# Performance work log

Hardware: AMD Instinct MI355X
Metric: run time of the kernel (lower is better)

The kernel has to match this reference:

```python
import jax, jax.numpy as jnp
import numpy as np

TEMPERATURE = 0.07
MSE_WEIGHT = 0.5
SUPCON_WEIGHT = 1.0
EPS = 1e-12  # F.normalize default eps

P_POS = 4000
P_NEG = 4000
NVOX = 32768
FEAT = 128


def setup_inputs() -> dict:
    key = jax.random.key(0)
    k1, k2, k3, k4, k5 = jax.random.split(key, 5)
    Zs = jax.random.normal(k1, (1, FEAT, NVOX), dtype=jnp.float32)
    pos_idx = jax.random.randint(k2, (P_POS,), 0, NVOX, dtype=jnp.int32)
    neg_idx = jax.random.randint(k3, (P_NEG,), 0, NVOX, dtype=jnp.int32)
    feature_diff = jax.random.normal(k4, (1, FEAT, 32, 32, 32), dtype=jnp.float32)
    input_diff = jax.random.normal(k5, (1, FEAT, 32, 32, 32), dtype=jnp.float32)
    return {"Zs": Zs, "pos_idx": pos_idx, "neg_idx": neg_idx,
            "feature_diff": feature_diff, "input_diff": input_diff}


def _l2_normalize_rows(x):
    # F.normalize(x, dim=1): x / max(||x||_2, eps)
    n = jnp.sqrt(jnp.sum(x * x, axis=1, keepdims=True))
    return x / jnp.maximum(n, EPS)


def _supcon_loss(Zs, pos_idx, neg_idx):
    feats = Zs[0].T                                   # [Nvox, F]
    pixels = jnp.concatenate([feats[pos_idx], feats[neg_idx]], axis=0)  # [N, F]
    n = pixels.shape[0]
    labels = jnp.concatenate([jnp.ones((P_POS,), jnp.int32),
                              jnp.zeros((P_NEG,), jnp.int32)])
    pixels = _l2_normalize_rows(pixels)
    dot = jnp.matmul(pixels, pixels.T) / TEMPERATURE  # [N, N]
    dot = _l2_normalize_rows(dot)                     # row-normalize the NxN matrix
    expm = jnp.exp(dot)
    class_mask = (labels[:, None] == labels[None, :]) & ~jnp.eye(n, dtype=bool)
    pos_term = expm * class_mask
    pos_term = jnp.where(pos_term == 0, 1.0, pos_term)
    denom = jnp.sum(expm * ~class_mask, axis=1) - jnp.diagonal(expm)  # [N]
    full_term = jnp.log(pos_term) - jnp.log(denom)[None, :]
    return -(1.0 / n) * jnp.sum(full_term)


def reference(Zs, pos_idx, neg_idx, feature_diff, input_diff):
    supcon = _supcon_loss(Zs, pos_idx, neg_idx)
    mse = jnp.mean((feature_diff - input_diff) ** 2)
    return SUPCON_WEIGHT * supcon + MSE_WEIGHT * mse
```

## Files before the change

### kernel.cpp

```cpp
#include <hip/hip_runtime.h>
#include <hip/hip_bf16.h>
#include <math.h>

typedef unsigned short u16;
typedef float  f32x4  __attribute__((ext_vector_type(4)));
typedef __bf16 bf16x8 __attribute__((ext_vector_type(8)));

#define NPOS   4000
#define LDP    136
#define TILE_CH 2176
#define MSE_N  4194304
#define GATHER_B 256
#define MSE_B    512
#define TLD    132

__device__ __forceinline__ void load_lds16(const void* g, void* l) {
  __builtin_amdgcn_global_load_lds(
      (const __attribute__((address_space(1))) unsigned int*)g,
      (__attribute__((address_space(3))) unsigned int*)l, 16, 0, 0);
}

__device__ __forceinline__ float bf2f(u16 h) {
  unsigned u = ((unsigned)h) << 16;
  return __builtin_bit_cast(float, u);
}

struct Args {
  const float* Zs; const int* pos; const int* neg;
  const float4* fd; const float4* idf;
  u16* Pc; u16* Prow; float* G; float* S;
  float* qpos; float* qneg; float* sdpos; float* sdneg;
  float* msepart; float* out;
};

__global__ __launch_bounds__(256) void prep_k(Args a) {
  __shared__ __align__(16) float tile[128 * TLD];
  __shared__ int mlist[1024];
  __shared__ int mcnt;
  int blk = blockIdx.x, tid = threadIdx.x;
  int wave = tid >> 6, lane = tid & 63;
  if (blk < GATHER_B) {
    int v0 = blk << 7;
    if (tid == 0) mcnt = 0;
    __syncthreads();
    {
      int rq = tid >> 5;
      int c4 = (tid & 31) << 2;
      #pragma unroll
      for (int p = 0; p < 16; ++p) {
        int f = p * 8 + rq;
        float4 v = *(const float4*)(a.Zs + ((size_t)f << 15) + v0 + c4);
        *(float4*)&tile[f * TLD + c4] = v;
      }
    }
    for (int k = 0; k < 4000; k += 256) {
      int i = k + tid;
      if (i < 4000) {
        unsigned dp = (unsigned)(a.pos[i] - v0);
        if (dp < 128u) { int m = atomicAdd(&mcnt, 1); mlist[m] = (i << 7) | dp; }
        unsigned dn = (unsigned)(a.neg[i] - v0);
        if (dn < 128u) { int m = atomicAdd(&mcnt, 1); mlist[m] = ((4096 + i) << 7) | dn; }
      }
    }
    __syncthreads();
    int nm = mcnt;
    for (int m = wave; m < nm; m += 4) {
      int e = mlist[m];
      int col = e >> 7, lv = e & 127;
      float x0 = tile[lane * TLD + lv];
      float x1 = tile[(lane + 64) * TLD + lv];
      float s = x0 * x0 + x1 * x1;
      #pragma unroll
      for (int o = 1; o < 64; o <<= 1) s += __shfl_xor(s, o, 64);
      float inv = 1.0f / fmaxf(sqrtf(s), 1e-12f);
      __hip_bfloat16 h0 = __float2bfloat16(x0 * inv);
      __hip_bfloat16 h1 = __float2bfloat16(x1 * inv);
      u16 b0 = *(u16*)&h0, b1 = *(u16*)&h1;
      a.Prow[(size_t)col * LDP + lane]      = b0;
      a.Prow[(size_t)col * LDP + lane + 64] = b1;
      size_t cbase = (size_t)(col >> 7) * (128 * LDP) + (col & 127);
      a.Pc[cbase + (size_t)lane * LDP]        = b0;
      a.Pc[cbase + (size_t)(lane + 64) * LDP] = b1;
    }
  } else if (blk < GATHER_B + MSE_B) {
    int b = blk - GATHER_B;
    float ms = 0.f;
    for (int idx = b * 256 + tid; idx < MSE_N / 4; idx += MSE_B * 256) {
      float4 u = a.fd[idx], w = a.idf[idx];
      float dx = u.x - w.x, dy = u.y - w.y, dz = u.z - w.z, dv = u.w - w.w;
      ms += dx * dx + dy * dy + dz * dz + dv * dv;
    }
    #pragma unroll
    for (int o = 1; o < 64; o <<= 1) ms += __shfl_xor(ms, o, 64);
    __shared__ float red[4];
    if (lane == 0) red[wave] = ms;
    __syncthreads();
    if (tid == 0) a.msepart[b] = red[0] + red[1] + red[2] + red[3];
  } else if (blk < GATHER_B + MSE_B + 2) {
    int ch = (blk == GATHER_B + MSE_B) ? 31 : 63;
    for (int e = tid; e < 128 * 96; e += 256) {
      int f = e / 96, c = 32 + e % 96;
      a.Pc[(size_t)ch * (128 * LDP) + (size_t)f * LDP + c] = 0;
    }
  } else {
    int b = blk - (GATHER_B + MSE_B + 2);
    float4 z = {0.f, 0.f, 0.f, 0.f};
    for (int i = b * 256 + tid; i < 8256; i += 512) ((float4*)a.G)[i] = z;
  }
}

__global__ __launch_bounds__(256) void syrk_k(Args a) {
  __shared__ __align__(16) u16 T0[128 * LDP];
  int blk = blockIdx.x, tid = threadIdx.x;
  int wave = tid >> 6, lane = tid & 63;
  int wm = (wave >> 1) << 6, wn = (wave & 1) << 6;
  int r = lane & 15, q = lane >> 4;
  int sf = tid >> 1, sh = tid & 1;
  float ssum = 0.f;
  f32x4 acc[4][4];
  #pragma unroll
  for (int x = 0; x < 4; ++x)
    #pragma unroll
    for (int y = 0; y < 4; ++y) {
      acc[x][y][0] = 0.f; acc[x][y][1] = 0.f; acc[x][y][2] = 0.f; acc[x][y][3] = 0.f;
    }
  for (int it = 0; it < 4; ++it) {
    const u16* g = a.Pc + (size_t)(blk * 4 + it) * (128 * LDP);
    #pragma unroll
    for (int k = 0; k < 9; ++k) {
      int cc = k * 256 + tid;
      if (cc < TILE_CH) load_lds16(g + cc * 8, &T0[cc * 8]);
    }
    __syncthreads();
    #pragma unroll
    for (int kk = 0; kk < 4; ++kk) {
      int k0 = kk * 32 + q * 8;
      bf16x8 af[4], bfr[4];
      #pragma unroll
      for (int t = 0; t < 4; ++t) {
        af[t]  = *(const bf16x8*)&T0[(wm + t * 16 + r) * LDP + k0];
        bfr[t] = *(const bf16x8*)&T0[(wn + t * 16 + r) * LDP + k0];
      }
      #pragma unroll
      for (int mt = 0; mt < 4; ++mt)
        #pragma unroll
        for (int nt = 0; nt < 4; ++nt)
          acc[mt][nt] = __builtin_amdgcn_mfma_f32_16x16x32_bf16(
              af[mt], bfr[nt], acc[mt][nt], 0, 0, 0);
    }
    {
      const u16* base = &T0[sf * LDP + sh * 64];
      #pragma unroll
      for (int vb = 0; vb < 8; ++vb) {
        bf16x8 v = *(const bf16x8*)&base[vb * 8];
        #pragma unroll
        for (int j = 0; j < 8; ++j) ssum += (float)v[j];
      }
    }
    __syncthreads();
  }
  float* Gf = a.G + (size_t)(blk >> 3) * 16384;
  #pragma unroll
  for (int mt = 0; mt < 4; ++mt)
    #pragma unroll
    for (int nt = 0; nt < 4; ++nt)
      #pragma unroll
      for (int reg = 0; reg < 4; ++reg) {
        int ar = wm + mt * 16 + q * 4 + reg;
        int bc = wn + nt * 16 + r;
        atomicAdd(&Gf[ar * 128 + bc], acc[mt][nt][reg]);
      }
  ssum += __shfl_xor(ssum, 1, 64);
  if (sh == 0) atomicAdd(&a.S[(blk >> 3) * 128 + sf], ssum);
}

__global__ __launch_bounds__(256) void quad_k(Args a) {
  __shared__ __align__(16) u16 T0[128 * LDP];
  __shared__ __align__(16) u16 T1[128 * LDP];
  __shared__ float Sl[256];
  __shared__ float qld[2][128];
  int cb = blockIdx.x & 63, set = blockIdx.x >> 6, tid = threadIdx.x;
  Sl[tid] = a.S[tid];
  const u16* gP = a.Prow + (size_t)cb * (128 * LDP);
  #pragma unroll
  for (int k = 0; k < 9; ++k) {
    int cc = k * 256 + tid;
    if (cc < TILE_CH) load_lds16(gP + cc * 8, &T1[cc * 8]);
  }
  {
    int f = tid >> 1, half = (tid & 1) * 64;
    const float4* gsrc = (const float4*)(a.G + (size_t)set * 16384 + f * 128 + half);
    #pragma unroll
    for (int j16 = 0; j16 < 16; ++j16) {
      float4 v = gsrc[j16];
      __hip_bfloat16 c0 = __float2bfloat16(v.x), c1 = __float2bfloat16(v.y);
      __hip_bfloat16 c2 = __float2bfloat16(v.z), c3 = __float2bfloat16(v.w);
      ushort4 pk = { *(u16*)&c0, *(u16*)&c1, *(u16*)&c2, *(u16*)&c3 };
      *(ushort4*)&T0[f * LDP + half + j16 * 4] = pk;
    }
  }
  __syncthreads();
  int wave = tid >> 6, lane = tid & 63;
  int wm = (wave >> 1) << 6, wn = (wave & 1) << 6;
  int r = lane & 15, q = lane >> 4;
  f32x4 acc[4][4];
  #pragma unroll
  for (int x = 0; x < 4; ++x)
    #pragma unroll
    for (int y = 0; y < 4; ++y) {
      acc[x][y][0] = 0.f; acc[x][y][1] = 0.f; acc[x][y][2] = 0.f; acc[x][y][3] = 0.f;
    }
  #pragma unroll
  for (int kk = 0; kk < 4; ++kk) {
    int k0 = kk * 32 + q * 8;
    bf16x8 af[4], bfr[4];
    #pragma unroll
    for (int t = 0; t < 4; ++t) {
      af[t]  = *(const bf16x8*)&T0[(wm + t * 16 + r) * LDP + k0];
      bfr[t] = *(const bf16x8*)&T1[(wn + t * 16 + r) * LDP + k0];
    }
    #pragma unroll
    for (int mt = 0; mt < 4; ++mt)
      #pragma unroll
      for (int nt = 0; nt < 4; ++nt)
        acc[mt][nt] = __builtin_amdgcn_mfma_f32_16x16x32_bf16(
            af[mt], bfr[nt], acc[mt][nt], 0, 0, 0);
  }
  float qv[4] = {0.f, 0.f, 0.f, 0.f};
  #pragma unroll
  for (int nt = 0; nt < 4; ++nt) {
    int il = wn + nt * 16 + r;
    #pragma unroll
    for (int mt = 0; mt < 4; ++mt) {
      const u16* pp = &T1[il * LDP + wm + mt * 16 + q * 4];
      #pragma unroll
      for (int reg = 0; reg < 4; ++reg)
        qv[nt] += acc[mt][nt][reg] * bf2f(pp[reg]);
    }
  }
  #pragma unroll
  for (int nt = 0; nt < 4; ++nt) {
    qv[nt] += __shfl_xor(qv[nt], 16, 64);
    qv[nt] += __shfl_xor(qv[nt], 32, 64);
  }
  int half = wm >> 6;
  if (q == 0) {
    #pragma unroll
    for (int nt = 0; nt < 4; ++nt) qld[half][wn + nt * 16 + r] = qv[nt];
  }
  __syncthreads();
  float* qarr = set ? a.qneg : a.qpos;
  if (tid < 128) qarr[cb * 128 + tid] = qld[0][tid] + qld[1][tid];
  if (set == 0) {
    int which = tid >> 7, sl = tid & 127;
    const float* Sv = &Sl[which * 128];
    float d = 0.f;
    #pragma unroll
    for (int fb = 0; fb < 16; ++fb) {
      const u16* pv = &T1[sl * LDP + fb * 8];
      #pragma unroll
      for (int j = 0; j < 8; ++j) d += Sv[fb * 8 + j] * bf2f(pv[j]);
    }
    (which ? a.sdneg : a.sdpos)[cb * 128 + sl] = d;
  }
}

__global__ __launch_bounds__(256) void final_k(Args a) {
  int tid = threadIdx.x;
  int wave = tid >> 6, lane = tid & 63;
  float lg = 0.f, sm = 0.f;
  for (int col = tid; col < 8192; col += 256) {
    bool isp = col < NPOS;
    bool isn = (col >= 4096) && (col < 4096 + NPOS);
    if (isp || isn) {
      float qp = a.qpos[col], qn = a.qneg[col];
      float c = 1.0f / sqrtf(qp + qn);
      float qo  = isp ? qn : qp;
      float sdo = isp ? a.sdneg[col] : a.sdpos[col];
      float sds = isp ? a.sdpos[col] : a.sdneg[col];
      float denom = 4000.0f + c * sdo + 0.5f * c * c * qo;
      lg += logf(denom);
      sm += c * (sds - 1.0f);
    }
  }
  float ms = a.msepart[tid] + a.msepart[tid + 256];
  #pragma unroll
  for (int o = 1; o < 64; o <<= 1) {
    lg += __shfl_xor(lg, o, 64);
    sm += __shfl_xor(sm, o, 64);
    ms += __shfl_xor(ms, o, 64);
  }
  __shared__ float redf[12];
  if (lane == 0) { redf[wave] = lg; redf[4 + wave] = sm; redf[8 + wave] = ms; }
  __syncthreads();
  if (tid == 0) {
    float lgs = redf[0] + redf[1] + redf[2] + redf[3];
    float sms = redf[4] + redf[5] + redf[6] + redf[7];
    float mss = redf[8] + redf[9] + redf[10] + redf[11];
    a.out[0] = lgs - sms * (1.0f / 8000.0f) + 0.5f * (mss * (1.0f / (float)MSE_N));
  }
}

extern "C" void kernel_launch(void* const* d_in, const int* in_sizes, int n_in,
                              void* d_out, int out_size, void* d_ws, size_t ws_size,
                              hipStream_t stream) {
  char* ws = (char*)d_ws;
  Args args;
  args.Zs  = (const float*)d_in[0];
  args.pos = (const int*)d_in[1];
  args.neg = (const int*)d_in[2];
  args.fd  = (const float4*)d_in[3];
  args.idf = (const float4*)d_in[4];
  args.out = (float*)d_out;

  args.Pc      = (u16*)(ws + 0);
  args.Prow    = (u16*)(ws + 2228224);
  args.G       = (float*)(ws + 4456448);
  args.S       = (float*)(ws + 4587520);
  args.qpos    = (float*)(ws + 4588544);
  args.qneg    = (float*)(ws + 4621312);
  args.sdpos   = (float*)(ws + 4654080);
  args.sdneg   = (float*)(ws + 4686848);
  args.msepart = (float*)(ws + 4719616);

  prep_k<<<GATHER_B + MSE_B + 4, 256, 0, stream>>>(args);
  syrk_k<<<16, 256, 0, stream>>>(args);
  quad_k<<<128, 256, 0, stream>>>(args);
  final_k<<<1, 256, 0, stream>>>(args);
}
```

Before: 133.5 us.

## Fuse syrk, quad and final kernels into one with atomic-counter grid sync

```diff
diff --git a/kernel.cpp b/kernel.cpp
--- a/kernel.cpp
+++ b/kernel.cpp
@@ -28,7 +28,7 @@
 struct Args {
   const float* Zs; const int* pos; const int* neg;
   const float4* fd; const float4* idf;
-  u16* Pc; u16* Prow; float* G; float* S;
+  u16* Pc; u16* Prow; float* G; float* S; unsigned* ctr;
   float* qpos; float* qneg; float* sdpos; float* sdneg;
   float* msepart; float* out;
 };
@@ -105,88 +105,102 @@
   } else {
     int b = blk - (GATHER_B + MSE_B + 2);
     float4 z = {0.f, 0.f, 0.f, 0.f};
-    for (int i = b * 256 + tid; i < 8256; i += 512) ((float4*)a.G)[i] = z;
-  }
-}
-
-__global__ __launch_bounds__(256) void syrk_k(Args a) {
+    for (int i = b * 256 + tid; i < 8258; i += 512) ((float4*)a.G)[i] = z;
+  }
+}
+
+__global__ __launch_bounds__(256) void solve_k(Args a) {
   __shared__ __align__(16) u16 T0[128 * LDP];
+  __shared__ __align__(16) u16 T1[128 * LDP];
+  __shared__ float Sl[256];
+  __shared__ float qld[2][128];
+  __shared__ int lastf;
   int blk = blockIdx.x, tid = threadIdx.x;
   int wave = tid >> 6, lane = tid & 63;
   int wm = (wave >> 1) << 6, wn = (wave & 1) << 6;
   int r = lane & 15, q = lane >> 4;
-  int sf = tid >> 1, sh = tid & 1;
-  float ssum = 0.f;
-  f32x4 acc[4][4];
-  #pragma unroll
-  for (int x = 0; x < 4; ++x)
-    #pragma unroll
-    for (int y = 0; y < 4; ++y) {
-      acc[x][y][0] = 0.f; acc[x][y][1] = 0.f; acc[x][y][2] = 0.f; acc[x][y][3] = 0.f;
-    }
-  for (int it = 0; it < 4; ++it) {
-    const u16* g = a.Pc + (size_t)(blk * 4 + it) * (128 * LDP);
-    #pragma unroll
-    for (int k = 0; k < 9; ++k) {
-      int cc = k * 256 + tid;
-      if (cc < TILE_CH) load_lds16(g + cc * 8, &T0[cc * 8]);
-    }
-    __syncthreads();
-    #pragma unroll
-    for (int kk = 0; kk < 4; ++kk) {
-      int k0 = kk * 32 + q * 8;
-      bf16x8 af[4], bfr[4];
-      #pragma unroll
-      for (int t = 0; t < 4; ++t) {
-        af[t]  = *(const bf16x8*)&T0[(wm + t * 16 + r) * LDP + k0];
-        bfr[t] = *(const bf16x8*)&T0[(wn + t * 16 + r) * LDP + k0];
-      }
-      #pragma unroll
-      for (int mt = 0; mt < 4; ++mt)
-        #pragma unroll
-        for (int nt = 0; nt < 4; ++nt)
-          acc[mt][nt] = __builtin_amdgcn_mfma_f32_16x16x32_bf16(
-              af[mt], bfr[nt], acc[mt][nt], 0, 0, 0);
-    }
-    {
-      const u16* base = &T0[sf * LDP + sh * 64];
-      #pragma unroll
-      for (int vb = 0; vb < 8; ++vb) {
-        bf16x8 v = *(const bf16x8*)&base[vb * 8];
-        #pragma unroll
-        for (int j = 0; j < 8; ++j) ssum += (float)v[j];
-      }
-    }
-    __syncthreads();
-  }
-  float* Gf = a.G + (size_t)(blk >> 3) * 16384;
-  #pragma unroll
-  for (int mt = 0; mt < 4; ++mt)
-    #pragma unroll
-    for (int nt = 0; nt < 4; ++nt)
-      #pragma unroll
-      for (int reg = 0; reg < 4; ++reg) {
-        int ar = wm + mt * 16 + q * 4 + reg;
-        int bc = wn + nt * 16 + r;
-        atomicAdd(&Gf[ar * 128 + bc], acc[mt][nt][reg]);
-      }
-  ssum += __shfl_xor(ssum, 1, 64);
-  if (sh == 0) atomicAdd(&a.S[(blk >> 3) * 128 + sf], ssum);
-}
-
-__global__ __launch_bounds__(256) void quad_k(Args a) {
-  __shared__ __align__(16) u16 T0[128 * LDP];
-  __shared__ __align__(16) u16 T1[128 * LDP];
-  __shared__ float Sl[256];
-  __shared__ float qld[2][128];
-  int cb = blockIdx.x & 63, set = blockIdx.x >> 6, tid = threadIdx.x;
-  Sl[tid] = a.S[tid];
+  int cb = blk & 63, set = blk >> 6;
+
   const u16* gP = a.Prow + (size_t)cb * (128 * LDP);
   #pragma unroll
   for (int k = 0; k < 9; ++k) {
     int cc = k * 256 + tid;
     if (cc < TILE_CH) load_lds16(gP + cc * 8, &T1[cc * 8]);
   }
+
+  if (blk < 16) {
+    int sf = tid >> 1, sh = tid & 1;
+    float ssum = 0.f;
+    f32x4 acc[4][4];
+    #pragma unroll
+    for (int x = 0; x < 4; ++x)
+      #pragma unroll
+      for (int y = 0; y < 4; ++y) {
+        acc[x][y][0] = 0.f; acc[x][y][1] = 0.f; acc[x][y][2] = 0.f; acc[x][y][3] = 0.f;
+      }
+    for (int it = 0; it < 4; ++it) {
+      const u16* g = a.Pc + (size_t)(blk * 4 + it) * (128 * LDP);
+      #pragma unroll
+      for (int k = 0; k < 9; ++k) {
+        int cc = k * 256 + tid;
+        if (cc < TILE_CH) load_lds16(g + cc * 8, &T0[cc * 8]);
+      }
+      __syncthreads();
+      #pragma unroll
+      for (int kk = 0; kk < 4; ++kk) {
+        int k0 = kk * 32 + q * 8;
+        bf16x8 af[4], bfr[4];
+        #pragma unroll
+        for (int t = 0; t < 4; ++t) {
+          af[t]  = *(const bf16x8*)&T0[(wm + t * 16 + r) * LDP + k0];
+          bfr[t] = *(const bf16x8*)&T0[(wn + t * 16 + r) * LDP + k0];
+        }
+        #pragma unroll
+        for (int mt = 0; mt < 4; ++mt)
+          #pragma unroll
+          for (int nt = 0; nt < 4; ++nt)
+            acc[mt][nt] = __builtin_amdgcn_mfma_f32_16x16x32_bf16(
+                af[mt], bfr[nt], acc[mt][nt], 0, 0, 0);
+      }
+      {
+        const u16* base = &T0[sf * LDP + sh * 64];
+        #pragma unroll
+        for (int vb = 0; vb < 8; ++vb) {
+          bf16x8 v = *(const bf16x8*)&base[vb * 8];
+          #pragma unroll
+          for (int j = 0; j < 8; ++j) ssum += (float)v[j];
+        }
+      }
+      __syncthreads();
+    }
+    float* Gf = a.G + (size_t)(blk >> 3) * 16384;
+    #pragma unroll
+    for (int mt = 0; mt < 4; ++mt)
+      #pragma unroll
+      for (int nt = 0; nt < 4; ++nt)
+        #pragma unroll
+        for (int reg = 0; reg < 4; ++reg) {
+          int ar = wm + mt * 16 + q * 4 + reg;
+          int bc = wn + nt * 16 + r;
+          atomicAdd(&Gf[ar * 128 + bc], acc[mt][nt][reg]);
+        }
+    ssum += __shfl_xor(ssum, 1, 64);
+    if (sh == 0) atomicAdd(&a.S[(blk >> 3) * 128 + sf], ssum);
+    __threadfence();
+    __syncthreads();
+    if (tid == 0)
+      __hip_atomic_fetch_add(&a.ctr[0], 1u, __ATOMIC_RELEASE,
+                             __HIP_MEMORY_SCOPE_AGENT);
+  }
+
+  if (tid == 0) {
+    while (__hip_atomic_load(&a.ctr[0], __ATOMIC_ACQUIRE,
+                             __HIP_MEMORY_SCOPE_AGENT) < 16u)
+      __builtin_amdgcn_s_sleep(8);
+  }
+  __syncthreads();
+
+  Sl[tid] = a.S[tid];
   {
     int f = tid >> 1, half = (tid & 1) * 64;
     const float4* gsrc = (const float4*)(a.G + (size_t)set * 16384 + f * 128 + half);
@@ -200,9 +214,6 @@
     }
   }
   __syncthreads();
-  int wave = tid >> 6, lane = tid & 63;
-  int wm = (wave >> 1) << 6, wn = (wave & 1) << 6;
-  int r = lane & 15, q = lane >> 4;
   f32x4 acc[4][4];
   #pragma unroll
   for (int x = 0; x < 4; ++x)
@@ -263,41 +274,47 @@
     }
     (which ? a.sdneg : a.sdpos)[cb * 128 + sl] = d;
   }
-}
-
-__global__ __launch_bounds__(256) void final_k(Args a) {
-  int tid = threadIdx.x;
-  int wave = tid >> 6, lane = tid & 63;
-  float lg = 0.f, sm = 0.f;
-  for (int col = tid; col < 8192; col += 256) {
-    bool isp = col < NPOS;
-    bool isn = (col >= 4096) && (col < 4096 + NPOS);
-    if (isp || isn) {
-      float qp = a.qpos[col], qn = a.qneg[col];
-      float c = 1.0f / sqrtf(qp + qn);
-      float qo  = isp ? qn : qp;
-      float sdo = isp ? a.sdneg[col] : a.sdpos[col];
-      float sds = isp ? a.sdpos[col] : a.sdneg[col];
-      float denom = 4000.0f + c * sdo + 0.5f * c * c * qo;
-      lg += logf(denom);
-      sm += c * (sds - 1.0f);
-    }
-  }
-  float ms = a.msepart[tid] + a.msepart[tid + 256];
-  #pragma unroll
-  for (int o = 1; o < 64; o <<= 1) {
-    lg += __shfl_xor(lg, o, 64);
-    sm += __shfl_xor(sm, o, 64);
-    ms += __shfl_xor(ms, o, 64);
-  }
-  __shared__ float redf[12];
-  if (lane == 0) { redf[wave] = lg; redf[4 + wave] = sm; redf[8 + wave] = ms; }
+
+  __threadfence();
   __syncthreads();
   if (tid == 0) {
-    float lgs = redf[0] + redf[1] + redf[2] + redf[3];
-    float sms = redf[4] + redf[5] + redf[6] + redf[7];
-    float mss = redf[8] + redf[9] + redf[10] + redf[11];
-    a.out[0] = lgs - sms * (1.0f / 8000.0f) + 0.5f * (mss * (1.0f / (float)MSE_N));
+    unsigned old = __hip_atomic_fetch_add(&a.ctr[1], 1u, __ATOMIC_ACQ_REL,
+                                          __HIP_MEMORY_SCOPE_AGENT);
+    lastf = (old == 127u);
+  }
+  __syncthreads();
+  if (lastf) {
+    float lg = 0.f, sm = 0.f;
+    for (int col = tid; col < 8192; col += 256) {
+      bool isp = col < NPOS;
+      bool isn = (col >= 4096) && (col < 4096 + NPOS);
+      if (isp || isn) {
+        float qp = a.qpos[col], qn = a.qneg[col];
+        float c = 1.0f / sqrtf(qp + qn);
+        float qo  = isp ? qn : qp;
+        float sdo = isp ? a.sdneg[col] : a.sdpos[col];
+        float sds = isp ? a.sdpos[col] : a.sdneg[col];
+        float denom = 4000.0f + c * sdo + 0.5f * c * c * qo;
+        lg += logf(denom);
+        sm += c * (sds - 1.0f);
+      }
+    }
+    float ms = a.msepart[tid] + a.msepart[tid + 256];
+    #pragma unroll
+    for (int o = 1; o < 64; o <<= 1) {
+      lg += __shfl_xor(lg, o, 64);
+      sm += __shfl_xor(sm, o, 64);
+      ms += __shfl_xor(ms, o, 64);
+    }
+    __shared__ float redf[12];
+    if (lane == 0) { redf[wave] = lg; redf[4 + wave] = sm; redf[8 + wave] = ms; }
+    __syncthreads();
+    if (tid == 0) {
+      float lgs = redf[0] + redf[1] + redf[2] + redf[3];
+      float sms = redf[4] + redf[5] + redf[6] + redf[7];
+      float mss = redf[8] + redf[9] + redf[10] + redf[11];
+      a.out[0] = lgs - sms * (1.0f / 8000.0f) + 0.5f * (mss * (1.0f / (float)MSE_N));
+    }
   }
 }
 
@@ -317,14 +334,13 @@
   args.Prow    = (u16*)(ws + 2228224);
   args.G       = (float*)(ws + 4456448);
   args.S       = (float*)(ws + 4587520);
-  args.qpos    = (float*)(ws + 4588544);
-  args.qneg    = (float*)(ws + 4621312);
-  args.sdpos   = (float*)(ws + 4654080);
-  args.sdneg   = (float*)(ws + 4686848);
-  args.msepart = (float*)(ws + 4719616);
+  args.ctr     = (unsigned*)(ws + 4588544);
+  args.qpos    = (float*)(ws + 4588576);
+  args.qneg    = (float*)(ws + 4621344);
+  args.sdpos   = (float*)(ws + 4654112);
+  args.sdneg   = (float*)(ws + 4686880);
+  args.msepart = (float*)(ws + 4719648);
 
   prep_k<<<GATHER_B + MSE_B + 4, 256, 0, stream>>>(args);
-  syrk_k<<<16, 256, 0, stream>>>(args);
-  quad_k<<<128, 256, 0, stream>>>(args);
-  final_k<<<1, 256, 0, stream>>>(args);
-}
+  solve_k<<<128, 256, 0, stream>>>(args);
+}
```

New measurement: 150.8 us. +13.0%, slower.
